# Optimization experiments

Measured on AMD Instinct MI355X. Metric: run time of the kernel, lower is better.

## Reference

```python
import jax, jax.numpy as jnp
import numpy as np

IN_F = 1024
HID = 1024
OUT_F = 1024


def setup_inputs() -> dict:
    key = jax.random.key(0)
    ks = jax.random.split(key, 6)
    B, S = 64, 512
    x = jax.random.normal(ks[0], (B, S, IN_F), dtype=jnp.float32)
    hidden_first = jnp.zeros((B, HID), dtype=jnp.float32)
    lim1 = 1.0 / np.sqrt(IN_F + HID)
    lim2 = 1.0 / np.sqrt(HID)
    W_ih = jax.random.uniform(ks[1], (HID, IN_F + HID), minval=-lim1, maxval=lim1, dtype=jnp.float32)
    b_ih = jax.random.uniform(ks[2], (HID,), minval=-lim1, maxval=lim1, dtype=jnp.float32)
    W_ho = jax.random.uniform(ks[3], (OUT_F, HID), minval=-lim2, maxval=lim2, dtype=jnp.float32)
    b_ho = jax.random.uniform(ks[4], (OUT_F,), minval=-lim2, maxval=lim2, dtype=jnp.float32)
    return {"x": x, "hidden_first": hidden_first, "W_ih": W_ih, "b_ih": b_ih, "W_ho": W_ho, "b_ho": b_ho}


def reference(x, hidden_first, W_ih, b_ih, W_ho, b_ho):
    # x: [B, S, F] -> time-major [S, B, F]
    xt = jnp.swapaxes(x, 0, 1)
    # Split in2hidden weight into input and hidden blocks to avoid per-step concat
    W_x = W_ih[:, :IN_F]   # [H, F]
    W_h = W_ih[:, IN_F:]   # [H, H]
    # Precompute input projections for all timesteps in one big GEMM
    x_proj = jnp.einsum('sbf,hf->sbh', xt, W_x) + b_ih  # [S, B, H]

    def step(h, xp):
        h_new = jnp.tanh(xp + h @ W_h.T)
        out_t = h_new @ W_ho.T + b_ho
        return h_new, out_t

    _, outs = jax.lax.scan(step, hidden_first, x_proj)  # outs: [S, B, O]
    return jnp.swapaxes(outs, 0, 1)  # [B, S, O]
```

## Files before the change

### kernel.cpp

```cpp
#include <hip/hip_runtime.h>
#include <stdint.h>

typedef __attribute__((ext_vector_type(8))) short short8_t;
typedef __attribute__((ext_vector_type(4))) float f32x4_t;

__device__ __forceinline__ unsigned short f2bf_u(float f) {
  unsigned int u = __float_as_uint(f);
  unsigned int r = (u + 0x7fff + ((u >> 16) & 1)) >> 16;
  return (unsigned short)r;
}
__device__ __forceinline__ float bf2f(unsigned short s) {
  return __uint_as_float(((unsigned int)s) << 16);
}
__device__ __forceinline__ short8_t pack8(float4 a, float4 b) {
  short8_t r;
  r[0]=(short)f2bf_u(a.x); r[1]=(short)f2bf_u(a.y); r[2]=(short)f2bf_u(a.z); r[3]=(short)f2bf_u(a.w);
  r[4]=(short)f2bf_u(b.x); r[5]=(short)f2bf_u(b.y); r[6]=(short)f2bf_u(b.z); r[7]=(short)f2bf_u(b.w);
  return r;
}
__device__ __forceinline__ void gl_lds16(const void* g, void* l) {
  __builtin_amdgcn_global_load_lds(
      (const __attribute__((address_space(1))) unsigned int*)g,
      (__attribute__((address_space(3))) unsigned int*)l, 16, 0, 0);
}

__global__ void k_prep_x(const float* __restrict__ src, unsigned short* __restrict__ dst) {
  int i = blockIdx.x * blockDim.x + threadIdx.x;
  if (i >= 4194304) return;
  const float4* s = (const float4*)src + (size_t)i * 2;
  float4 a = s[0], b = s[1];
  *(short8_t*)(dst + (size_t)i * 8) = pack8(a, b);
}

__global__ void k_prep_w(const float* __restrict__ Wih, const float* __restrict__ Who,
                         unsigned short* __restrict__ Wxbf, unsigned short* __restrict__ Whobf,
                         int* __restrict__ flags) {
  int tid = blockIdx.x * blockDim.x + threadIdx.x;
  if (tid < 131072) {
    int n = tid >> 7, c = tid & 127;
    const float* s = Wih + (size_t)n * 2048 + c * 8;
    float4 a = *(const float4*)s, b = *(const float4*)(s + 4);
    *(short8_t*)(Wxbf + (size_t)n * 1024 + c * 8) = pack8(a, b);
  } else {
    int j = tid - 131072;
    int n = j >> 7, c = j & 127;
    const float* s = Who + (size_t)n * 1024 + c * 8;
    float4 a = *(const float4*)s, b = *(const float4*)(s + 4);
    *(short8_t*)(Whobf + (size_t)n * 1024 + c * 8) = pack8(a, b);
  }
  if (tid < 32768) flags[tid] = 0;
}

template <bool OUT_BF16>
__global__ __launch_bounds__(256, 2) void k_gemm_bt(
    const unsigned short* __restrict__ A, const unsigned short* __restrict__ Bw,
    const float* __restrict__ bias, void* __restrict__ Cout) {
  constexpr int K = 1024, N = 1024;
  __shared__ unsigned short sm[8192];
  const int tid = threadIdx.x;
  const int wave = tid >> 6, lane = tid & 63;
  const int tm = blockIdx.y * 128, tn = blockIdx.x * 128;
  const int wm = wave >> 1, wn = wave & 1;

  f32x4_t acc[4][4];
#pragma unroll
  for (int i = 0; i < 4; i++)
#pragma unroll
    for (int j = 0; j < 4; j++) acc[i][j] = (f32x4_t){0.f, 0.f, 0.f, 0.f};

  char* ldsA = (char*)sm;
  char* ldsB = (char*)sm + 8192;
  const int cc = ((lane & 3) ^ ((lane >> 3) & 3)) * 8;
  const int rs = lane >> 2;

  for (int k0 = 0; k0 < K; k0 += 32) {
    __syncthreads();
#pragma unroll
    for (int c = 0; c < 2; c++) {
      int r0 = c * 64 + wave * 16;
      int r = r0 + rs;
      gl_lds16(A + (size_t)(tm + r) * K + (k0 + cc), ldsA + r0 * 64);
      gl_lds16(Bw + (size_t)(tn + r) * K + (k0 + cc), ldsB + r0 * 64);
    }
    __builtin_amdgcn_s_waitcnt(0);
    __syncthreads();

    short8_t af[4], bf[4];
#pragma unroll
    for (int mt = 0; mt < 4; mt++) {
      int r = wm * 64 + mt * 16 + (lane & 15);
      int slot = (((lane >> 4) ^ (((lane & 15) >> 1) & 3))) * 16;
      af[mt] = *(const short8_t*)(ldsA + r * 64 + slot);
    }
#pragma unroll
    for (int nt = 0; nt < 4; nt++) {
      int r = wn * 64 + nt * 16 + (lane & 15);
      int slot = (((lane >> 4) ^ (((lane & 15) >> 1) & 3))) * 16;
      bf[nt] = *(const short8_t*)(ldsB + r * 64 + slot);
    }
#pragma unroll
    for (int mt = 0; mt < 4; mt++)
#pragma unroll
      for (int nt = 0; nt < 4; nt++)
        acc[mt][nt] = __builtin_amdgcn_mfma_f32_16x16x32_bf16(af[mt], bf[nt], acc[mt][nt], 0, 0, 0);
  }

#pragma unroll
  for (int nt = 0; nt < 4; nt++) {
    int n = tn + wn * 64 + nt * 16 + (lane & 15);
    float bs = bias[n];
#pragma unroll
    for (int mt = 0; mt < 4; mt++) {
      int rowb = tm + wm * 64 + mt * 16 + ((lane >> 4) << 2);
      f32x4_t v = acc[mt][nt];
#pragma unroll
      for (int q = 0; q < 4; q++) {
        float o = v[q] + bs;
        size_t off = (size_t)(rowb + q) * N + n;
        if (OUT_BF16) ((unsigned short*)Cout)[off] = f2bf_u(o);
        else          ((float*)Cout)[off] = o;
      }
    }
  }
}

__global__ __launch_bounds__(256, 1) void k_rnn(
    const float* __restrict__ Wih, const float* __restrict__ h0,
    const unsigned short* __restrict__ xproj, unsigned short* __restrict__ Hall,
    unsigned short* __restrict__ hx, int* __restrict__ flags) {
  const int bid = blockIdx.x;
  const int g = (bid & 7) >> 1;
  const int rank = ((bid >> 3) << 1) | (bid & 1);
  const int tid = threadIdx.x;
  const int wave = tid >> 6, lane = tid & 63;
  const int nw = rank * 64 + wave * 16;
  const int b0 = g * 16;

  __shared__ unsigned short hs[16][1032];
  __shared__ unsigned short hsOut[16][68];

  short8_t bfrag[32];
  {
    const int n = nw + (lane & 15);
    const float* wrow = Wih + (size_t)n * 2048 + 1024 + ((lane >> 4) * 8);
#pragma unroll
    for (int kt = 0; kt < 32; kt++) {
      float4 f0 = *(const float4*)(wrow + kt * 32);
      float4 f1 = *(const float4*)(wrow + kt * 32 + 4);
      bfrag[kt] = pack8(f0, f1);
    }
  }

  const int row = tid >> 4, c16 = tid & 15;
  int* gflags = flags + g * 16 * 512;

  for (int t = 0; t < 512; t++) {
    unsigned short xr[4];
#pragma unroll
    for (int q = 0; q < 4; q++) {
      int b = b0 + ((lane >> 4) << 2) + q;
      xr[q] = xproj[((size_t)b * 512 + t) * 1024 + nw + (lane & 15)];
    }

    if (t > 0) {
      if (tid < 16 && tid != rank) {
        while (__hip_atomic_load(&gflags[tid * 512 + (t - 1)],
                                 __ATOMIC_RELAXED, __HIP_MEMORY_SCOPE_AGENT) == 0) {}
      }
      __syncthreads();
      *(unsigned long long*)&hs[row][(rank * 16 + c16) * 4] =
          *(const unsigned long long*)&hsOut[row][c16 * 4];
      const int slot = (t - 1) & 1;
      unsigned long long v[16];
#pragma unroll
      for (int j = 0; j < 16; j++) {
        if (j == rank) continue;
        size_t off = ((size_t)(slot * 4 + g) * 16 + row) * 1024 + j * 64 + c16 * 4;
        v[j] = __hip_atomic_load((unsigned long long*)(hx + off),
                                 __ATOMIC_RELAXED, __HIP_MEMORY_SCOPE_AGENT);
      }
#pragma unroll
      for (int j = 0; j < 16; j++) {
        if (j == rank) continue;
        *(unsigned long long*)&hs[row][(j * 16 + c16) * 4] = v[j];
      }
    } else {
      const float* s = h0 + (size_t)(b0 + row) * 1024 + c16 * 8;
#pragma unroll
      for (int j = 0; j < 8; j++) {
        float4 a = *(const float4*)(s + j * 128);
        float4 b = *(const float4*)(s + j * 128 + 4);
        *(short8_t*)&hs[row][c16 * 8 + j * 128] = pack8(a, b);
      }
    }
    __syncthreads();

    f32x4_t acc0 = {0.f, 0.f, 0.f, 0.f}, acc1 = {0.f, 0.f, 0.f, 0.f};
    {
      const char* abase = (const char*)&hs[lane & 15][0] + ((lane >> 4) * 16);
#pragma unroll
      for (int kt = 0; kt < 32; kt += 2) {
        short8_t a0 = *(const short8_t*)(abase + kt * 64);
        acc0 = __builtin_amdgcn_mfma_f32_16x16x32_bf16(a0, bfrag[kt], acc0, 0, 0, 0);
        short8_t a1 = *(const short8_t*)(abase + (kt + 1) * 64);
        acc1 = __builtin_amdgcn_mfma_f32_16x16x32_bf16(a1, bfrag[kt + 1], acc1, 0, 0, 0);
      }
    }

#pragma unroll
    for (int q = 0; q < 4; q++) {
      int bl = ((lane >> 4) << 2) + q;
      float p = acc0[q] + acc1[q] + bf2f(xr[q]);
      float e = __expf(2.0f * p);
      float th = 1.0f - 2.0f / (e + 1.0f);
      hsOut[bl][wave * 16 + (lane & 15)] = f2bf_u(th);
    }
    __syncthreads();

    {
      unsigned long long vv = *(const unsigned long long*)&hsOut[row][c16 * 4];
      size_t hall_off = ((size_t)(b0 + row) * 512 + t) * 1024 + rank * 64 + c16 * 4;
      *(unsigned long long*)(Hall + hall_off) = vv;
      const int slot = t & 1;
      size_t hx_off = ((size_t)(slot * 4 + g) * 16 + row) * 1024 + rank * 64 + c16 * 4;
      __hip_atomic_store((unsigned long long*)(hx + hx_off), vv,
                         __ATOMIC_RELAXED, __HIP_MEMORY_SCOPE_AGENT);
    }
    __syncthreads();

    if (tid == 0)
      __hip_atomic_store(&gflags[rank * 512 + t], 1,
                         __ATOMIC_RELAXED, __HIP_MEMORY_SCOPE_AGENT);
  }
}

extern "C" void kernel_launch(void* const* d_in, const int* in_sizes, int n_in,
                              void* d_out, int out_size, void* d_ws, size_t ws_size,
                              hipStream_t stream) {
  const float* x   = (const float*)d_in[0];
  const float* h0  = (const float*)d_in[1];
  const float* Wih = (const float*)d_in[2];
  const float* bih = (const float*)d_in[3];
  const float* Who = (const float*)d_in[4];
  const float* bho = (const float*)d_in[5];

  char* ws = (char*)d_ws;
  unsigned short* Xbf   = (unsigned short*)ws;
  unsigned short* Hall  = (unsigned short*)ws;
  unsigned short* xproj = (unsigned short*)(ws + 67108864);
  unsigned short* Wxbf  = (unsigned short*)(ws + 134217728);
  unsigned short* Whobf = (unsigned short*)(ws + 136314880);
  int*            flags = (int*)(ws + 138412032);
  unsigned short* hx    = (unsigned short*)(ws + 138543104);

  k_prep_x<<<16384, 256, 0, stream>>>(x, Xbf);
  k_prep_w<<<1024, 256, 0, stream>>>(Wih, Who, Wxbf, Whobf, flags);
  k_gemm_bt<true ><<<dim3(8, 256), 256, 0, stream>>>(Xbf, Wxbf, bih, (void*)xproj);
  k_rnn<<<64, 256, 0, stream>>>(Wih, h0, xproj, Hall, hx, flags);
  k_gemm_bt<false><<<dim3(8, 256), 256, 0, stream>>>(Hall, Whobf, bho, d_out);
}
```

Before: 1.806 ms.

## Replace per-step flag handshake with timestamp-tagged hidden-state exchange lines

The recurrent kernel no longer uses separate flag words plus two block barriers per timestep to publish hidden-state slices between workgroups. Each thread now writes its slice together with the step number inside one 16-byte store. Consumers poll these lines directly with system-coherent loads until every tag matches, which removes the flag round trip and the extra barriers from the serial critical path. The risk is relying on 16-byte stores being observed atomically. Polling also becomes heavier because all lanes spin on the data lines.

```diff
diff --git a/kernel.cpp b/kernel.cpp
--- a/kernel.cpp
+++ b/kernel.cpp
@@ -3,6 +3,7 @@
 
 typedef __attribute__((ext_vector_type(8))) short short8_t;
 typedef __attribute__((ext_vector_type(4))) float f32x4_t;
+typedef __attribute__((ext_vector_type(4))) unsigned int u32x4_t;
 
 __device__ __forceinline__ unsigned short f2bf_u(float f) {
   unsigned int u = __float_as_uint(f);
@@ -34,7 +35,7 @@
 
 __global__ void k_prep_w(const float* __restrict__ Wih, const float* __restrict__ Who,
                          unsigned short* __restrict__ Wxbf, unsigned short* __restrict__ Whobf,
-                         int* __restrict__ flags) {
+                         u32x4_t* __restrict__ hx2) {
   int tid = blockIdx.x * blockDim.x + threadIdx.x;
   if (tid < 131072) {
     int n = tid >> 7, c = tid & 127;
@@ -48,7 +49,10 @@
     float4 a = *(const float4*)s, b = *(const float4*)(s + 4);
     *(short8_t*)(Whobf + (size_t)n * 1024 + c * 8) = pack8(a, b);
   }
-  if (tid < 32768) flags[tid] = 0;
+  if (tid < 32768) {
+    u32x4_t z; z[0] = 0; z[1] = 0; z[2] = 0; z[3] = 0;
+    hx2[tid] = z;
+  }
 }
 
 template <bool OUT_BF16>
@@ -127,7 +131,7 @@
 __global__ __launch_bounds__(256, 1) void k_rnn(
     const float* __restrict__ Wih, const float* __restrict__ h0,
     const unsigned short* __restrict__ xproj, unsigned short* __restrict__ Hall,
-    unsigned short* __restrict__ hx, int* __restrict__ flags) {
+    char* __restrict__ hx2) {
   const int bid = blockIdx.x;
   const int g = (bid & 7) >> 1;
   const int rank = ((bid >> 3) << 1) | (bid & 1);
@@ -152,7 +156,8 @@
   }
 
   const int row = tid >> 4, c16 = tid & 15;
-  int* gflags = flags + g * 16 * 512;
+  const char* hxb = hx2 + g * 65536;
+  const unsigned voffc = (unsigned)(row * 256 + c16 * 16);
 
   for (int t = 0; t < 512; t++) {
     unsigned short xr[4];
@@ -163,26 +168,37 @@
     }
 
     if (t > 0) {
-      if (tid < 16 && tid != rank) {
-        while (__hip_atomic_load(&gflags[tid * 512 + (t - 1)],
-                                 __ATOMIC_RELAXED, __HIP_MEMORY_SCOPE_AGENT) == 0) {}
-      }
-      __syncthreads();
       *(unsigned long long*)&hs[row][(rank * 16 + c16) * 4] =
           *(const unsigned long long*)&hsOut[row][c16 * 4];
-      const int slot = (t - 1) & 1;
-      unsigned long long v[16];
-#pragma unroll
-      for (int j = 0; j < 16; j++) {
-        if (j == rank) continue;
-        size_t off = ((size_t)(slot * 4 + g) * 16 + row) * 1024 + j * 64 + c16 * 4;
-        v[j] = __hip_atomic_load((unsigned long long*)(hx + off),
-                                 __ATOMIC_RELAXED, __HIP_MEMORY_SCOPE_AGENT);
-      }
-#pragma unroll
-      for (int j = 0; j < 16; j++) {
-        if (j == rank) continue;
-        *(unsigned long long*)&hs[row][(j * 16 + c16) * 4] = v[j];
+      const unsigned tg = (unsigned)t;
+      const unsigned so = ((t - 1) & 1) ? 262144u : 0u;
+      unsigned done = 1u << rank;
+      u32x4_t r[16];
+#pragma unroll
+      for (int j = 0; j < 16; j++) { r[j][0] = 0; r[j][1] = 0; r[j][2] = 0; r[j][3] = 0; }
+      while (done != 0xFFFFu) {
+#pragma unroll
+        for (int j = 0; j < 16; j++) {
+          if (!((done >> j) & 1)) {
+            asm volatile("global_load_dwordx4 %0, %1, %2 sc0 sc1"
+                         : "=v"(r[j])
+                         : "v"(so + (unsigned)(j << 12) + voffc), "s"(hxb)
+                         : "memory");
+          }
+        }
+        asm volatile("s_waitcnt vmcnt(0)"
+                     : "+v"(r[0]), "+v"(r[1]), "+v"(r[2]), "+v"(r[3]),
+                       "+v"(r[4]), "+v"(r[5]), "+v"(r[6]), "+v"(r[7]),
+                       "+v"(r[8]), "+v"(r[9]), "+v"(r[10]), "+v"(r[11]),
+                       "+v"(r[12]), "+v"(r[13]), "+v"(r[14]), "+v"(r[15]));
+#pragma unroll
+        for (int j = 0; j < 16; j++) {
+          if (!((done >> j) & 1) && r[j][1] == tg && r[j][3] == tg) {
+            *(unsigned long long*)&hs[row][(j * 16 + c16) * 4] =
+                (unsigned long long)r[j][0] | ((unsigned long long)r[j][2] << 32);
+            done |= 1u << j;
+          }
+        }
       }
     } else {
       const float* s = h0 + (size_t)(b0 + row) * 1024 + c16 * 8;
@@ -221,16 +237,14 @@
       unsigned long long vv = *(const unsigned long long*)&hsOut[row][c16 * 4];
       size_t hall_off = ((size_t)(b0 + row) * 512 + t) * 1024 + rank * 64 + c16 * 4;
       *(unsigned long long*)(Hall + hall_off) = vv;
-      const int slot = t & 1;
-      size_t hx_off = ((size_t)(slot * 4 + g) * 16 + row) * 1024 + rank * 64 + c16 * 4;
-      __hip_atomic_store((unsigned long long*)(hx + hx_off), vv,
-                         __ATOMIC_RELAXED, __HIP_MEMORY_SCOPE_AGENT);
-    }
-    __syncthreads();
-
-    if (tid == 0)
-      __hip_atomic_store(&gflags[rank * 512 + t], 1,
-                         __ATOMIC_RELAXED, __HIP_MEMORY_SCOPE_AGENT);
+      u32x4_t line;
+      line[0] = (unsigned)vv;         line[1] = (unsigned)(t + 1);
+      line[2] = (unsigned)(vv >> 32); line[3] = (unsigned)(t + 1);
+      const unsigned sow = (t & 1) ? 262144u : 0u;
+      asm volatile("global_store_dwordx4 %0, %1, %2 sc0 sc1"
+                   :: "v"(sow + (unsigned)(rank << 12) + voffc), "v"(line), "s"(hxb)
+                   : "memory");
+    }
   }
 }
 
@@ -250,12 +264,11 @@
   unsigned short* xproj = (unsigned short*)(ws + 67108864);
   unsigned short* Wxbf  = (unsigned short*)(ws + 134217728);
   unsigned short* Whobf = (unsigned short*)(ws + 136314880);
-  int*            flags = (int*)(ws + 138412032);
-  unsigned short* hx    = (unsigned short*)(ws + 138543104);
+  char*           hx2   = ws + 138412032;
 
   k_prep_x<<<16384, 256, 0, stream>>>(x, Xbf);
-  k_prep_w<<<1024, 256, 0, stream>>>(Wih, Who, Wxbf, Whobf, flags);
+  k_prep_w<<<1024, 256, 0, stream>>>(Wih, Who, Wxbf, Whobf, (u32x4_t*)hx2);
   k_gemm_bt<true ><<<dim3(8, 256), 256, 0, stream>>>(Xbf, Wxbf, bih, (void*)xproj);
-  k_rnn<<<64, 256, 0, stream>>>(Wih, h0, xproj, Hall, hx, flags);
+  k_rnn<<<64, 256, 0, stream>>>(Wih, h0, xproj, Hall, hx2);
   k_gemm_bt<false><<<dim3(8, 256), 256, 0, stream>>>(Hall, Whobf, bho, d_out);
 }
```

Measured after the change: 1.955 ms. +8.3%, slower.
